# Kernel optimization log

Hardware: AMD Instinct MI355X
Metric: run time of the kernel (lower is better)

The kernel has to match this reference:

```python
import jax, jax.numpy as jnp
import numpy as np

D = 512      # emb_size
H = 8        # attention heads
E = 8        # num experts
HID = 512    # expert MLP hidden (assumed StandardExpert = 2-layer MLP)
NTOK = 8192  # 8*1024 tokens
W_IMP = 0.01


def setup_inputs() -> dict:
    key = jax.random.key(0)
    ks = jax.random.split(key, 16)
    f = lambda i, shape, s=0.02: (jax.random.normal(ks[i], shape, jnp.float32) * s)
    return {
        "x": jax.random.normal(ks[0], (8, 1024, D), jnp.float32),
        "q": jax.random.normal(ks[1], (NTOK, D), jnp.float32),
        "Wq": f(2, (D, D)), "bq": jnp.zeros((D,), jnp.float32),
        "Wk": f(3, (D, D)), "bk": jnp.zeros((D,), jnp.float32),
        "Wv": f(4, (D, D)), "bv": jnp.zeros((D,), jnp.float32),
        "Wo": f(5, (D, D)), "bo": jnp.zeros((D,), jnp.float32),
        "gate_W": f(6, (D, E)), "gate_b": jnp.zeros((E,), jnp.float32),
        "W1": f(7, (E, D, HID)), "b1": jnp.zeros((E, HID), jnp.float32),
        "W2": f(8, (E, HID, D)), "b2": jnp.zeros((E, D), jnp.float32),
        "top": 2,
    }


def _cross_att(xf, q, Wq, bq, Wk, bk, Wv, bv, Wo, bo):
    # seq_len == 1 on both sides after unsqueeze(1) in the torch code
    N, d = xf.shape
    dh = d // H
    Q = (xf @ Wq + bq).reshape(N, H, dh)
    K = (q @ Wk + bk).reshape(N, H, dh)
    V = (q @ Wv + bv).reshape(N, H, dh)
    scores = jnp.sum(Q * K, axis=-1, keepdims=True) / jnp.sqrt(jnp.float32(dh))  # [N,H,1]
    w = jax.nn.softmax(scores, axis=-1)  # trivially ones (single key), kept for fidelity
    att = (w * V).reshape(N, d)
    return att @ Wo + bo


def reference(x, q, Wq, bq, Wk, bk, Wv, bv, Wo, bo, gate_W, gate_b, W1, b1, W2, b2, top):
    x_shape = x.shape
    xf = x.reshape(-1, x_shape[-1])  # [N, D]
    att = _cross_att(xf, q, Wq, bq, Wk, bk, Wv, bv, Wo, bo)
    gate_logits = att @ gate_W + gate_b
    gate_prob = jax.nn.softmax(gate_logits, axis=-1)  # [N, E] (eval mode: no noise)
    top_w, top_i = jax.lax.top_k(gate_prob, top)       # [N, top]
    top_w = jax.nn.softmax(top_w, axis=-1)
    # combine weights per expert: comb[n,e] = sum_k top_w[n,k] * [top_i[n,k]==e]
    comb = jnp.sum(top_w[..., None] * jax.nn.one_hot(top_i, E, dtype=xf.dtype), axis=1)  # [N, E]
    y = jnp.zeros_like(xf)
    for e in range(E):  # fixed small expert loop; dense compute + mask-combine
        h = jax.nn.relu(xf @ W1[e] + b1[e])
        ye = h @ W2[e] + b2[e]
        y = y + comb[:, e:e + 1] * ye
    importance = gate_prob.sum(axis=0)  # [E]
    # torch.std uses ddof=1
    importance_loss = W_IMP * (jnp.std(importance, ddof=1) / jnp.mean(importance)) ** 2
    return y.reshape(x_shape), gate_prob, importance_loss
```

## Files before the change

### kernel.cpp

```cpp
#include <hip/hip_runtime.h>
#include <math.h>
#include <stdint.h>

#define NTOK 8192
#define DIM  512
#define NEXP 8
#define HIDN 512
#define BM 128
#define BN 128
#define BK 32
#define NT  (DIM / BK)
#define MAXRB 72
#define SLOTS (MAXRB*BM)
#define GBLK (NTOK/16)

typedef _Float16 f16;
typedef __attribute__((ext_vector_type(4))) _Float16 f16x4;
typedef __attribute__((ext_vector_type(8))) _Float16 f16x8;
typedef __attribute__((ext_vector_type(4))) float    f32x4;

__device__ __forceinline__ void gl2lds16(const void* g, void* l) {
  __builtin_amdgcn_global_load_lds(
      (const __attribute__((address_space(1))) unsigned int*)(g),
      (__attribute__((address_space(3))) unsigned int*)(l), 16, 0, 0);
}

__global__ __launch_bounds__(256) void k_prep(
    const float* __restrict__ x, f16* __restrict__ xh,
    const float* __restrict__ W1, const float* __restrict__ W2,
    f16* __restrict__ W1t, f16* __restrict__ W2t,
    const float* __restrict__ Wo, const float* __restrict__ gW,
    double* __restrict__ G1) {
  const int bx = blockIdx.x, tid = threadIdx.x;
  if (bx < 4096) {
    int i4 = (bx * 256 + tid) * 4;
    float4 v = *(const float4*)(x + i4);
    f16x4 o; o.x = (_Float16)v.x; o.y = (_Float16)v.y; o.z = (_Float16)v.z; o.w = (_Float16)v.w;
    *(f16x4*)(xh + i4) = o;
  } else if (bx < 8192) {
    __shared__ float t[32][33];
    int idx = bx - 4096;
    int z = idx >> 8, rem = idx & 255;
    int k0 = (rem >> 4) * 32, n0 = (rem & 15) * 32;
    const float* src = (z < 8 ? W1 : W2) + (size_t)(z & 7) * DIM * DIM;
    f16* dst = (z < 8 ? W1t : W2t) + (size_t)(z & 7) * DIM * DIM;
    int tx = tid & 31, ty = tid >> 5;
    for (int r = ty; r < 32; r += 8) t[r][tx] = src[(size_t)(k0 + r) * DIM + n0 + tx];
    __syncthreads();
    for (int r = ty; r < 32; r += 8) dst[(size_t)(n0 + r) * DIM + k0 + tx] = (f16)t[tx][r];
  } else {
    int out = (bx - 8192) * 4 + (tid >> 6);
    int lane = tid & 63;
    int d = out >> 3, e = out & 7;
    double acc = 0.0;
#pragma unroll
    for (int j = 0; j < 8; j++) {
      int k = j * 64 + lane;
      acc += (double)Wo[d * DIM + k] * (double)gW[k * NEXP + e];
    }
#pragma unroll
    for (int off = 32; off; off >>= 1) acc += __shfl_xor(acc, off, 64);
    if (lane == 0) G1[out] = acc;
  }
}

__global__ void k_foldB(const float* __restrict__ Wv, const double* __restrict__ G1,
                        float* __restrict__ Wg, const float* __restrict__ bv,
                        const float* __restrict__ bo, const float* __restrict__ gW,
                        const float* __restrict__ gb, double* __restrict__ bg) {
  int lane = threadIdx.x & 63;
  if (blockIdx.x == 1024) {
    int w = threadIdx.x >> 6;
    for (int e = w; e < NEXP; e += 4) {
      double acc = 0.0;
#pragma unroll
      for (int j = 0; j < 8; j++) {
        int d = j * 64 + lane;
        acc += (double)bv[d] * G1[d * NEXP + e] + (double)bo[d] * (double)gW[d * NEXP + e];
      }
#pragma unroll
      for (int off = 32; off; off >>= 1) acc += __shfl_xor(acc, off, 64);
      if (lane == 0) bg[e] = acc + (double)gb[e];
    }
    return;
  }
  int out = blockIdx.x * 4 + (threadIdx.x >> 6);
  int d = out >> 3, e = out & 7;
  double acc = 0.0;
#pragma unroll
  for (int j = 0; j < 8; j++) {
    int k = j * 64 + lane;
    acc += (double)Wv[d * DIM + k] * G1[k * NEXP + e];
  }
#pragma unroll
  for (int off = 32; off; off >>= 1) acc += __shfl_xor(acc, off, 64);
  if (lane == 0) Wg[out] = (float)acc;
}

__global__ __launch_bounds__(256) void k_gate(
    const float* __restrict__ q, const float* __restrict__ Wg,
    const double* __restrict__ bg, float* __restrict__ gp_out,
    int* __restrict__ e1a, int* __restrict__ e2a,
    float* __restrict__ w1a, float* __restrict__ w2a,
    int* __restrict__ r1a, int* __restrict__ r2a, int* __restrict__ hist,
    float* __restrict__ gpsum) {
  __shared__ float qs[16 * 513];
  __shared__ float ps[16][8];
  __shared__ int cnt[16];
  const int tid = threadIdx.x;
  const int tok0 = blockIdx.x * 16;

  for (int i = tid; i < 16 * 512; i += 256) {
    int r = i >> 9, c = i & 511;
    qs[r * 513 + c] = q[(size_t)(tok0 + r) * DIM + c];
  }
  if (tid < 16) cnt[tid] = 0;
  __syncthreads();

  const int e = tid & 7;
  const int half = (tid >> 3) & 1;
  const int tl = tid >> 4;
  const float* qrow = qs + tl * 513 + half * 256;
  const float* wcol = Wg + half * 256 * NEXP + e;

  double a0 = 0, a1 = 0, a2 = 0, a3 = 0;
#pragma unroll 4
  for (int j = 0; j < 256; j += 4) {
    a0 += (double)qrow[j]     * (double)wcol[(size_t)j * NEXP];
    a1 += (double)qrow[j + 1] * (double)wcol[(size_t)(j + 1) * NEXP];
    a2 += (double)qrow[j + 2] * (double)wcol[(size_t)(j + 2) * NEXP];
    a3 += (double)qrow[j + 3] * (double)wcol[(size_t)(j + 3) * NEXP];
  }
  double acc = (a0 + a1) + (a2 + a3);
  acc += __shfl_xor(acc, 8, 64);

  double l = acc + bg[e];
  double m = l;
#pragma unroll
  for (int off = 1; off < 8; off <<= 1) m = fmax(m, __shfl_xor(m, off, 64));
  float ex = expf((float)(l - m));
  float s = ex;
#pragma unroll
  for (int off = 1; off < 8; off <<= 1) s += __shfl_xor(s, off, 64);
  float pf = ex / s;
  int tok = tok0 + tl;
  if (half == 0) { gp_out[(size_t)tok * NEXP + e] = pf; ps[tl][e] = pf; }

  double v1 = l; int i1 = e;
#pragma unroll
  for (int off = 1; off < 8; off <<= 1) {
    double ov = __shfl_xor(v1, off, 64);
    int oi = __shfl_xor(i1, off, 64);
    if (ov > v1 || (ov == v1 && oi < i1)) { v1 = ov; i1 = oi; }
  }
  double v2 = (e == i1) ? -1e300 : l; int i2 = e;
#pragma unroll
  for (int off = 1; off < 8; off <<= 1) {
    double ov = __shfl_xor(v2, off, 64);
    int oi = __shfl_xor(i2, off, 64);
    if (ov > v2 || (ov == v2 && oi < i2)) { v2 = ov; i2 = oi; }
  }
  float p1 = __shfl(pf, (tl << 4) + i1, 64);
  float p2 = __shfl(pf, (tl << 4) + i2, 64);
  if (e == 0 && half == 0) {
    float ev = expf(p2 - p1);
    float iw = 1.0f / (1.0f + ev);
    e1a[tok] = i1; e2a[tok] = i2;
    w1a[tok] = iw; w2a[tok] = ev * iw;
    r1a[tok] = atomicAdd(&cnt[i1], 1);
    r2a[tok] = atomicAdd(&cnt[8 + i2], 1);
  }
  __syncthreads();
  if (tid < 16) hist[blockIdx.x * 16 + tid] = cnt[tid];
  if (tid < 8) {
    float ssum = 0.f;
#pragma unroll
    for (int r = 0; r < 16; r++) ssum += ps[r][tid];
    gpsum[blockIdx.x * 8 + tid] = ssum;
  }
}

__global__ __launch_bounds__(1024) void k_scan2(const int* __restrict__ hist,
                                                int* __restrict__ blockbase,
                                                int* __restrict__ aoff,
                                                int* __restrict__ counts,
                                                int* __restrict__ toks,
                                                const float* __restrict__ gpsum,
                                                float* __restrict__ loss) {
  __shared__ int tot[16];
  __shared__ int s_ao[16];
  __shared__ double imp[8];
  const int c = threadIdx.x >> 6;
  const int l = threadIdx.x & 63;
  int v[GBLK / 64];
  int s = 0;
#pragma unroll
  for (int j = 0; j < GBLK / 64; j++) {
    v[j] = hist[((l * (GBLK / 64) + j) << 4) + c];
    s += v[j];
  }
  int incl = s;
#pragma unroll
  for (int off = 1; off < 64; off <<= 1) {
    int t = __shfl_up(incl, off, 64);
    if (l >= off) incl += t;
  }
  int run = incl - s;
#pragma unroll
  for (int j = 0; j < GBLK / 64; j++) {
    blockbase[((l * (GBLK / 64) + j) << 4) + c] = run;
    run += v[j];
  }
  if (l == 63) tot[c] = incl;
  __syncthreads();
  if (threadIdx.x == 0) {
    int o0 = 0, o1 = 0;
    for (int e = 0; e < NEXP; e++) {
      counts[e] = tot[e];
      aoff[e] = o0; s_ao[e] = o0; o0 += (tot[e] + BM - 1) / BM * BM;
      counts[8 + e] = tot[8 + e];
      aoff[9 + e] = o1; s_ao[8 + e] = o1; o1 += (tot[8 + e] + BM - 1) / BM * BM;
    }
    aoff[8] = o0; aoff[17] = o1;
  }
  __syncthreads();
  const int cnt_c = tot[c];
  const int padded = (cnt_c + BM - 1) / BM * BM;
  const int base = ((c >> 3) ? SLOTS : 0) + s_ao[c];
  for (int sidx = cnt_c + l; sidx < padded; sidx += 64)
    toks[base + sidx] = 0;
  if (c < 8) {
    double a = 0.0;
#pragma unroll
    for (int j = 0; j < GBLK / 64; j++)
      a += (double)gpsum[(size_t)(l + j * 64) * 8 + c];
#pragma unroll
    for (int off = 32; off; off >>= 1) a += __shfl_xor(a, off, 64);
    if (l == 0) imp[c] = a;
  }
  __syncthreads();
  if (threadIdx.x == 0) {
    double mn = 0.0;
    for (int e = 0; e < 8; e++) mn += imp[e];
    mn *= (1.0 / 8.0);
    double var = 0.0;
    for (int e = 0; e < 8; e++) { double d = imp[e] - mn; var += d * d; }
    var *= (1.0 / 7.0);
    double r = sqrt(var) / mn;
    loss[0] = (float)(0.01 * r * r);
  }
}

__global__ void k_scatter2(const int* __restrict__ e1a, const int* __restrict__ e2a,
                           const float* __restrict__ w1a, const float* __restrict__ w2a,
                           const int* __restrict__ r1a, const int* __restrict__ r2a,
                           const int* __restrict__ blockbase, const int* __restrict__ aoff,
                           int* __restrict__ toks, float* __restrict__ wsl) {
  int n = blockIdx.x * 256 + threadIdx.x;
  int blk = n >> 4;
  int e1 = e1a[n];
  int slot = aoff[e1] + blockbase[(blk << 4) + e1] + r1a[n];
  toks[slot] = n; wsl[slot] = w1a[n];
  int e2 = e2a[n];
  slot = SLOTS + aoff[9 + e2] + blockbase[(blk << 4) + 8 + e2] + r2a[n];
  toks[slot] = n; wsl[slot] = w2a[n];
}

template <int MODE>
__global__ __launch_bounds__(256) void k_expert(
    const f16* __restrict__ Asrc, const f16* __restrict__ Wt,
    const float* __restrict__ bias, const int* __restrict__ toks,
    const float* __restrict__ wsl, const int* __restrict__ aoff,
    const int* __restrict__ counts, f16* __restrict__ Hout,
    float* __restrict__ y) {
  const int klist = (MODE == 0) ? blockIdx.z : (MODE == 2 ? 1 : 0);
  const int* ao = aoff + klist * 9;
  const int slot0 = blockIdx.x * BM;
  if (slot0 >= ao[8]) return;
  int e = 0;
#pragma unroll
  for (int t = 1; t <= 7; t++) if (slot0 >= ao[t]) e = t;

  const int n0 = blockIdx.y * BN;
  const int tid = threadIdx.x, lane = tid & 63, wid = tid >> 6;

  __shared__ __align__(16) f16 As[2][BM * BK];
  __shared__ __align__(16) f16 Bs[2][BN * BK];

  const int srow = wid * 16 + (lane >> 2);
  const int scol = (lane & 3) * 8;
  const f16* arow[2];
  const f16* brow[2];
  int loff[2];
#pragma unroll
  for (int rnd = 0; rnd < 2; rnd++) {
    int r = srow + rnd * 64;
    if (MODE == 0) {
      int tk = toks[klist * SLOTS + slot0 + r];
      arow[rnd] = Asrc + (size_t)tk * DIM + scol;
    } else {
      arow[rnd] = Asrc + (size_t)(klist * SLOTS + slot0 + r) * HIDN + scol;
    }
    brow[rnd] = Wt + ((size_t)e * DIM + n0 + r) * DIM + scol;
    loff[rnd] = (wid * 16 + rnd * 64) * BK;
  }

  f32x4 acc[4][4] = {};
  const int wr = wid >> 1, wc = wid & 1;
  const int fr = lane & 15, kb = (lane >> 4) * 8;

#define STAGE(buf, ks)                                  \
  {                                                     \
    _Pragma("unroll")                                   \
    for (int rnd = 0; rnd < 2; rnd++) {                 \
      gl2lds16(arow[rnd] + (ks), As[buf] + loff[rnd]);  \
      gl2lds16(brow[rnd] + (ks), Bs[buf] + loff[rnd]);  \
    }                                                   \
  }

  STAGE(0, 0);
#pragma unroll 2
  for (int t = 0; t < NT; t++) {
    const int cur = t & 1;
    if (t + 1 < NT) {
      STAGE(cur ^ 1, (t + 1) * BK);
      asm volatile("s_waitcnt vmcnt(4)" ::: "memory");
    } else {
      asm volatile("s_waitcnt vmcnt(0)" ::: "memory");
    }
    __builtin_amdgcn_sched_barrier(0);
    __builtin_amdgcn_s_barrier();
    asm volatile("" ::: "memory");
    __builtin_amdgcn_sched_barrier(0);

    f16x8 af[4], bf[4];
#pragma unroll
    for (int m = 0; m < 4; m++)
      af[m] = *(const f16x8*)(As[cur] + (wr * 64 + m * 16 + fr) * BK + kb);
#pragma unroll
    for (int n = 0; n < 4; n++)
      bf[n] = *(const f16x8*)(Bs[cur] + (wc * 64 + n * 16 + fr) * BK + kb);
#pragma unroll
    for (int m = 0; m < 4; m++)
#pragma unroll
      for (int n = 0; n < 4; n++)
        acc[m][n] = __builtin_amdgcn_mfma_f32_16x16x32_f16(af[m], bf[n], acc[m][n], 0, 0, 0);

    asm volatile("s_waitcnt lgkmcnt(0)" ::: "memory");
    __builtin_amdgcn_sched_barrier(0);
    __builtin_amdgcn_s_barrier();
    asm volatile("" ::: "memory");
    __builtin_amdgcn_sched_barrier(0);
  }
#undef STAGE

  float bcol[4];
#pragma unroll
  for (int n = 0; n < 4; n++)
    bcol[n] = bias[e * ((MODE == 0) ? HIDN : DIM) + n0 + wc * 64 + n * 16 + fr];

  if (MODE == 0) {
#pragma unroll
    for (int m = 0; m < 4; m++)
#pragma unroll
      for (int r4 = 0; r4 < 4; r4++) {
        int slot = slot0 + wr * 64 + m * 16 + (lane >> 4) * 4 + r4;
#pragma unroll
        for (int n = 0; n < 4; n++) {
          int col = n0 + wc * 64 + n * 16 + fr;
          float v = acc[m][n][r4] + bcol[n];
          Hout[(size_t)(klist * SLOTS + slot) * HIDN + col] = (f16)fmaxf(v, 0.f);
        }
      }
  } else {
    const int vend = ao[e] + counts[klist * 8 + e];
#pragma unroll
    for (int m = 0; m < 4; m++)
#pragma unroll
      for (int r4 = 0; r4 < 4; r4++) {
        int slot = slot0 + wr * 64 + m * 16 + (lane >> 4) * 4 + r4;
        if (slot < vend) {
          int tk = toks[klist * SLOTS + slot];
          float w = wsl[klist * SLOTS + slot];
#pragma unroll
          for (int n = 0; n < 4; n++) {
            int col = n0 + wc * 64 + n * 16 + fr;
            float v = (acc[m][n][r4] + bcol[n]) * w;
            size_t oi = (size_t)tk * DIM + col;
            if (MODE == 1) y[oi] = v;
            else y[oi] += v;
          }
        }
      }
  }
}

extern "C" void kernel_launch(void* const* d_in, const int* in_sizes, int n_in,
                              void* d_out, int out_size, void* d_ws, size_t ws_size,
                              hipStream_t stream) {
  const float* x  = (const float*)d_in[0];
  const float* q  = (const float*)d_in[1];
  const float* Wv = (const float*)d_in[6];
  const float* bv = (const float*)d_in[7];
  const float* Wo = (const float*)d_in[8];
  const float* bo = (const float*)d_in[9];
  const float* gW = (const float*)d_in[10];
  const float* gb = (const float*)d_in[11];
  const float* W1 = (const float*)d_in[12];
  const float* b1 = (const float*)d_in[13];
  const float* W2 = (const float*)d_in[14];
  const float* b2 = (const float*)d_in[15];

  float* out = (float*)d_out;
  float* y_out = out;
  float* gp_out = out + (size_t)NTOK * DIM;
  float* loss_out = gp_out + (size_t)NTOK * NEXP;

  uint8_t* w = (uint8_t*)d_ws;
  size_t o = 0;
  auto alloc = [&](size_t bytes) -> void* {
    void* p = w + o;
    o = (o + bytes + 255) & ~(size_t)255;
    return p;
  };
  f16* xh      = (f16*)alloc((size_t)NTOK * DIM * 2);
  f16* W1t     = (f16*)alloc((size_t)NEXP * DIM * HIDN * 2);
  f16* W2t     = (f16*)alloc((size_t)NEXP * DIM * HIDN * 2);
  f16* Hbuf    = (f16*)alloc((size_t)2 * SLOTS * HIDN * 2);
  double* G1   = (double*)alloc((size_t)DIM * NEXP * 8);
  float* Wg    = (float*)alloc((size_t)DIM * NEXP * 4);
  double* bg   = (double*)alloc(NEXP * 8);
  int* e1a     = (int*)alloc(NTOK * 4);
  int* e2a     = (int*)alloc(NTOK * 4);
  float* w1a   = (float*)alloc(NTOK * 4);
  float* w2a   = (float*)alloc(NTOK * 4);
  int* r1a     = (int*)alloc(NTOK * 4);
  int* r2a     = (int*)alloc(NTOK * 4);
  int* hist    = (int*)alloc((size_t)GBLK * 16 * 4);
  int* bbase   = (int*)alloc((size_t)GBLK * 16 * 4);
  float* gpsum = (float*)alloc((size_t)GBLK * 8 * 4);
  int* counts  = (int*)alloc(16 * 4);
  int* aoff    = (int*)alloc(18 * 4);
  int* toks    = (int*)alloc((size_t)2 * SLOTS * 4);
  float* wsl   = (float*)alloc((size_t)2 * SLOTS * 4);
  (void)ws_size; (void)in_sizes; (void)n_in; (void)out_size;

  k_prep<<<9216, 256, 0, stream>>>(x, xh, W1, W2, W1t, W2t, Wo, gW, G1);
  k_foldB<<<1025, 256, 0, stream>>>(Wv, G1, Wg, bv, bo, gW, gb, bg);
  k_gate<<<GBLK, 256, 0, stream>>>(q, Wg, bg, gp_out, e1a, e2a, w1a, w2a, r1a, r2a, hist, gpsum);
  k_scan2<<<1, 1024, 0, stream>>>(hist, bbase, aoff, counts, toks, gpsum, loss_out);
  k_scatter2<<<NTOK / 256, 256, 0, stream>>>(e1a, e2a, w1a, w2a, r1a, r2a, bbase, aoff, toks, wsl);
  k_expert<0><<<dim3(MAXRB, 4, 2), 256, 0, stream>>>(xh, W1t, b1, toks, wsl, aoff, counts,
                                                     Hbuf, nullptr);
  k_expert<1><<<dim3(MAXRB, 4, 1), 256, 0, stream>>>(Hbuf, W2t, b2, toks, wsl, aoff, counts,
                                                     nullptr, y_out);
  k_expert<2><<<dim3(MAXRB, 4, 1), 256, 0, stream>>>(Hbuf, W2t, b2, toks, wsl, aoff, counts,
                                                     nullptr, y_out);
}
```

Before: 119.4 us.

## Fuse routing scan and scatter into one kernel; simplify expert GEMM barriers

Merges the single-block prefix scan and the token scatter into one k_route kernel. Each of 32 blocks recomputes the per-expert block-base scan into shared memory and then scatters its own 256 tokens. Block 0 alone writes the global offsets, the padding and the importance loss. This drops a kernel launch and the global blockbase round trip, at the cost of doing the scan redundantly in every block. Separately, the expert GEMM main loop replaces the hand-placed vmcnt/lgkmcnt waits, sched_barriers and unroll-2 pragma with a plain __syncthreads per iteration, which may change how well loads overlap with MFMA work.

Result: faster. 113.1 us (-5.3%).

```diff
diff --git a/kernel.cpp b/kernel.cpp
--- a/kernel.cpp
+++ b/kernel.cpp
@@ -180,13 +180,15 @@
   }
 }
 
-__global__ __launch_bounds__(1024) void k_scan2(const int* __restrict__ hist,
-                                                int* __restrict__ blockbase,
-                                                int* __restrict__ aoff,
-                                                int* __restrict__ counts,
-                                                int* __restrict__ toks,
-                                                const float* __restrict__ gpsum,
-                                                float* __restrict__ loss) {
+__global__ __launch_bounds__(1024) void k_route(
+    const int* __restrict__ hist,
+    const int* __restrict__ e1a, const int* __restrict__ e2a,
+    const float* __restrict__ w1a, const float* __restrict__ w2a,
+    const int* __restrict__ r1a, const int* __restrict__ r2a,
+    int* __restrict__ aoff, int* __restrict__ counts,
+    int* __restrict__ toks, float* __restrict__ wsl,
+    const float* __restrict__ gpsum, float* __restrict__ loss) {
+  __shared__ int bb[GBLK][16];
   __shared__ int tot[16];
   __shared__ int s_ao[16];
   __shared__ double imp[8];
@@ -208,62 +210,67 @@
   int run = incl - s;
 #pragma unroll
   for (int j = 0; j < GBLK / 64; j++) {
-    blockbase[((l * (GBLK / 64) + j) << 4) + c] = run;
+    bb[l * (GBLK / 64) + j][c] = run;
     run += v[j];
   }
   if (l == 63) tot[c] = incl;
   __syncthreads();
   if (threadIdx.x == 0) {
     int o0 = 0, o1 = 0;
+#pragma unroll
     for (int e = 0; e < NEXP; e++) {
-      counts[e] = tot[e];
-      aoff[e] = o0; s_ao[e] = o0; o0 += (tot[e] + BM - 1) / BM * BM;
-      counts[8 + e] = tot[8 + e];
-      aoff[9 + e] = o1; s_ao[8 + e] = o1; o1 += (tot[8 + e] + BM - 1) / BM * BM;
-    }
-    aoff[8] = o0; aoff[17] = o1;
+      s_ao[e] = o0;     o0 += (tot[e] + BM - 1) / BM * BM;
+      s_ao[8 + e] = o1; o1 += (tot[8 + e] + BM - 1) / BM * BM;
+    }
+    s_ao[8] = s_ao[8];
+    if (blockIdx.x == 0) {
+      int p0 = 0, p1 = 0;
+#pragma unroll
+      for (int e = 0; e < NEXP; e++) {
+        counts[e] = tot[e];         aoff[e] = p0;     p0 += (tot[e] + BM - 1) / BM * BM;
+        counts[8 + e] = tot[8 + e]; aoff[9 + e] = p1; p1 += (tot[8 + e] + BM - 1) / BM * BM;
+      }
+      aoff[8] = p0; aoff[17] = p1;
+    }
   }
   __syncthreads();
-  const int cnt_c = tot[c];
-  const int padded = (cnt_c + BM - 1) / BM * BM;
-  const int base = ((c >> 3) ? SLOTS : 0) + s_ao[c];
-  for (int sidx = cnt_c + l; sidx < padded; sidx += 64)
-    toks[base + sidx] = 0;
-  if (c < 8) {
-    double a = 0.0;
-#pragma unroll
-    for (int j = 0; j < GBLK / 64; j++)
-      a += (double)gpsum[(size_t)(l + j * 64) * 8 + c];
-#pragma unroll
-    for (int off = 32; off; off >>= 1) a += __shfl_xor(a, off, 64);
-    if (l == 0) imp[c] = a;
-  }
-  __syncthreads();
-  if (threadIdx.x == 0) {
-    double mn = 0.0;
-    for (int e = 0; e < 8; e++) mn += imp[e];
-    mn *= (1.0 / 8.0);
-    double var = 0.0;
-    for (int e = 0; e < 8; e++) { double d = imp[e] - mn; var += d * d; }
-    var *= (1.0 / 7.0);
-    double r = sqrt(var) / mn;
-    loss[0] = (float)(0.01 * r * r);
-  }
-}
-
-__global__ void k_scatter2(const int* __restrict__ e1a, const int* __restrict__ e2a,
-                           const float* __restrict__ w1a, const float* __restrict__ w2a,
-                           const int* __restrict__ r1a, const int* __restrict__ r2a,
-                           const int* __restrict__ blockbase, const int* __restrict__ aoff,
-                           int* __restrict__ toks, float* __restrict__ wsl) {
-  int n = blockIdx.x * 256 + threadIdx.x;
-  int blk = n >> 4;
-  int e1 = e1a[n];
-  int slot = aoff[e1] + blockbase[(blk << 4) + e1] + r1a[n];
-  toks[slot] = n; wsl[slot] = w1a[n];
-  int e2 = e2a[n];
-  slot = SLOTS + aoff[9 + e2] + blockbase[(blk << 4) + 8 + e2] + r2a[n];
-  toks[slot] = n; wsl[slot] = w2a[n];
+  if (blockIdx.x == 0) {
+    const int cnt_c = tot[c];
+    const int padded = (cnt_c + BM - 1) / BM * BM;
+    const int base = ((c >> 3) ? SLOTS : 0) + s_ao[c];
+    for (int sidx = cnt_c + l; sidx < padded; sidx += 64)
+      toks[base + sidx] = 0;
+    if (c < 8) {
+      double a = 0.0;
+#pragma unroll
+      for (int j = 0; j < GBLK / 64; j++)
+        a += (double)gpsum[(size_t)(l + j * 64) * 8 + c];
+#pragma unroll
+      for (int off = 32; off; off >>= 1) a += __shfl_xor(a, off, 64);
+      if (l == 0) imp[c] = a;
+    }
+    __syncthreads();
+    if (threadIdx.x == 0) {
+      double mn = 0.0;
+      for (int e = 0; e < 8; e++) mn += imp[e];
+      mn *= (1.0 / 8.0);
+      double var = 0.0;
+      for (int e = 0; e < 8; e++) { double d = imp[e] - mn; var += d * d; }
+      var *= (1.0 / 7.0);
+      double r = sqrt(var) / mn;
+      loss[0] = (float)(0.01 * r * r);
+    }
+  }
+  if (threadIdx.x < 256) {
+    int n = blockIdx.x * 256 + threadIdx.x;
+    int blk = n >> 4;
+    int e1 = e1a[n];
+    int slot = s_ao[e1] + bb[blk][e1] + r1a[n];
+    toks[slot] = n; wsl[slot] = w1a[n];
+    int e2 = e2a[n];
+    slot = SLOTS + s_ao[8 + e2] + bb[blk][8 + e2] + r2a[n];
+    toks[slot] = n; wsl[slot] = w2a[n];
+  }
 }
 
 template <int MODE>
@@ -319,20 +326,10 @@
   }
 
   STAGE(0, 0);
-#pragma unroll 2
+  __syncthreads();
   for (int t = 0; t < NT; t++) {
     const int cur = t & 1;
-    if (t + 1 < NT) {
-      STAGE(cur ^ 1, (t + 1) * BK);
-      asm volatile("s_waitcnt vmcnt(4)" ::: "memory");
-    } else {
-      asm volatile("s_waitcnt vmcnt(0)" ::: "memory");
-    }
-    __builtin_amdgcn_sched_barrier(0);
-    __builtin_amdgcn_s_barrier();
-    asm volatile("" ::: "memory");
-    __builtin_amdgcn_sched_barrier(0);
-
+    if (t + 1 < NT) STAGE(cur ^ 1, (t + 1) * BK);
     f16x8 af[4], bf[4];
 #pragma unroll
     for (int m = 0; m < 4; m++)
@@ -345,12 +342,7 @@
 #pragma unroll
       for (int n = 0; n < 4; n++)
         acc[m][n] = __builtin_amdgcn_mfma_f32_16x16x32_f16(af[m], bf[n], acc[m][n], 0, 0, 0);
-
-    asm volatile("s_waitcnt lgkmcnt(0)" ::: "memory");
-    __builtin_amdgcn_sched_barrier(0);
-    __builtin_amdgcn_s_barrier();
-    asm volatile("" ::: "memory");
-    __builtin_amdgcn_sched_barrier(0);
+    __syncthreads();
   }
 #undef STAGE
 
@@ -437,7 +429,6 @@
   int* r1a     = (int*)alloc(NTOK * 4);
   int* r2a     = (int*)alloc(NTOK * 4);
   int* hist    = (int*)alloc((size_t)GBLK * 16 * 4);
-  int* bbase   = (int*)alloc((size_t)GBLK * 16 * 4);
   float* gpsum = (float*)alloc((size_t)GBLK * 8 * 4);
   int* counts  = (int*)alloc(16 * 4);
   int* aoff    = (int*)alloc(18 * 4);
@@ -448,8 +439,8 @@
   k_prep<<<9216, 256, 0, stream>>>(x, xh, W1, W2, W1t, W2t, Wo, gW, G1);
   k_foldB<<<1025, 256, 0, stream>>>(Wv, G1, Wg, bv, bo, gW, gb, bg);
   k_gate<<<GBLK, 256, 0, stream>>>(q, Wg, bg, gp_out, e1a, e2a, w1a, w2a, r1a, r2a, hist, gpsum);
-  k_scan2<<<1, 1024, 0, stream>>>(hist, bbase, aoff, counts, toks, gpsum, loss_out);
-  k_scatter2<<<NTOK / 256, 256, 0, stream>>>(e1a, e2a, w1a, w2a, r1a, r2a, bbase, aoff, toks, wsl);
+  k_route<<<NTOK / 256, 1024, 0, stream>>>(hist, e1a, e2a, w1a, w2a, r1a, r2a,
+                                           aoff, counts, toks, wsl, gpsum, loss_out);
   k_expert<0><<<dim3(MAXRB, 4, 2), 256, 0, stream>>>(xh, W1t, b1, toks, wsl, aoff, counts,
                                                      Hbuf, nullptr);
   k_expert<1><<<dim3(MAXRB, 4, 1), 256, 0, stream>>>(Hbuf, W2t, b2, toks, wsl, aoff, counts,
```
